# Optimization experiments

Measured on AMD Instinct MI355X. Metric: run time of the kernel, lower is better.

## Reference

```python
import jax, jax.numpy as jnp
import numpy as np

N = 100000      # nodes
E = 1600000     # edges
D = 128         # embedding_size (num_heads=1)
L = 4           # num_layers
NEG_SLOPE_ATT = 0.2    # GATConv attention LeakyReLU
NEG_SLOPE_ACT = 0.01   # nn.LeakyReLU default
LN_EPS = 1e-5


def leaky(x, s):
    return jnp.where(x > 0, x, s * x)


def layer_norm(x, gamma, beta):
    mu = jnp.mean(x, axis=-1, keepdims=True)
    var = jnp.mean(jnp.square(x - mu), axis=-1, keepdims=True)
    return (x - mu) * jax.lax.rsqrt(var + LN_EPS) * gamma + beta


def gat_conv(x, src, dst, W, a_src, a_dst, b):
    # PyG GATConv, heads=1, add_self_loops=False, no edge features
    h = x @ W                                  # [N, D]
    alpha_src = h @ a_src                      # [N]
    alpha_dst = h @ a_dst                      # [N]
    e = leaky(alpha_src[src] + alpha_dst[dst], NEG_SLOPE_ATT)   # [E]
    # softmax over incoming edges of each destination node
    m = jax.ops.segment_max(e, dst, num_segments=N)             # [N]
    ex = jnp.exp(e - m[dst])
    denom = jax.ops.segment_sum(ex, dst, num_segments=N)        # [N]
    alpha = ex / (denom[dst] + 1e-16)                           # [E]
    out = jax.ops.segment_sum(alpha[:, None] * h[src], dst, num_segments=N)
    return out + b


def setup_inputs() -> dict:
    key = jax.random.key(0)
    ks = jax.random.split(key, 12)
    x = jax.random.normal(ks[0], (N, D), dtype=jnp.float32)
    edge_index = jax.random.randint(ks[1], (2, E), 0, N, dtype=jnp.int32)
    s = 0.05
    return {
        "x": x,
        "edge_index": edge_index,
        "W_in": jax.random.normal(ks[2], (D, D), dtype=jnp.float32) * s,
        "b_in": jnp.zeros((D,), dtype=jnp.float32),
        "Wl": jax.random.normal(ks[3], (L, D, D), dtype=jnp.float32) * s,
        "att_src": jax.random.normal(ks[4], (L, D), dtype=jnp.float32) * s,
        "att_dst": jax.random.normal(ks[5], (L, D), dtype=jnp.float32) * s,
        "bias_l": jnp.zeros((L, D), dtype=jnp.float32),
        "gamma": jnp.ones((L, D), dtype=jnp.float32),
        "beta": jnp.zeros((L, D), dtype=jnp.float32),
    }


def reference(x, edge_index, W_in, b_in, Wl, att_src, att_dst, bias_l, gamma, beta):
    src, dst = edge_index[0], edge_index[1]
    h = leaky(x @ W_in + b_in, NEG_SLOPE_ACT)
    for i in range(L):
        h = gat_conv(h, src, dst, Wl[i], att_src[i], att_dst[i], bias_l[i])
        h = layer_norm(h, gamma[i], beta[i])
        h = leaky(h, NEG_SLOPE_ACT)
        # dropout p=0.3 is identity in eval mode; pooling undefined in source -> identity
    return h
```

## Files before the change

### kernel.cpp

```cpp
#include <hip/hip_runtime.h>
#include <hip/hip_fp16.h>
#include <math.h>

#define NN 100000
#define EE 1600000
#define DD 128
#define NBUCK 196
#define NBLKP 196
#define EPB 8192

typedef _Float16 f16;
typedef f16 f16x8 __attribute__((ext_vector_type(8)));
typedef float f32x4 __attribute__((ext_vector_type(4)));
typedef int int32x4 __attribute__((ext_vector_type(4)));

__device__ float llvm_amdgcn_raw_buffer_load_fp32(int32x4 srsrc, int voffset, int soffset,
                                                  int aux) __asm("llvm.amdgcn.raw.buffer.load.f32");

#define LDA 136
#define WCHUNKS 2304
#define WCOPY 2176

__global__ __launch_bounds__(256) void part_hist_k(const int* __restrict__ dst, int* __restrict__ bcnt) {
    __shared__ int lc[NBUCK];
    int t = threadIdx.x, blk = blockIdx.x;
    if (t < NBUCK) lc[t] = 0;
    __syncthreads();
    int e0 = blk * EPB;
    for (int i = t; i < EPB; i += 256) {
        int e = e0 + i;
        if (e < EE) atomicAdd(&lc[dst[e] >> 9], 1);
    }
    __syncthreads();
    if (t < NBUCK) bcnt[t * NBLKP + blk] = lc[t];
}

__global__ __launch_bounds__(256) void scanBB_k(const int* __restrict__ bcnt, int* __restrict__ ebase,
                                                int* __restrict__ btot) {
    __shared__ int sh[256];
    int t = threadIdx.x, b = blockIdx.x;
    int c = (t < NBLKP) ? bcnt[b * NBLKP + t] : 0;
    sh[t] = c;
    __syncthreads();
    for (int off = 1; off < 256; off <<= 1) {
        int v = (t >= off) ? sh[t - off] : 0;
        __syncthreads();
        sh[t] += v;
        __syncthreads();
    }
    if (t < NBLKP) ebase[b * NBLKP + t] = sh[t] - c;
    if (t == 255) btot[b] = sh[255];
}

__global__ __launch_bounds__(256) void scanBT_k(const int* __restrict__ btot, int* __restrict__ bstart,
                                                int* __restrict__ offsets) {
    __shared__ int sh[256];
    int t = threadIdx.x;
    int c = (t < NBUCK) ? btot[t] : 0;
    sh[t] = c;
    __syncthreads();
    for (int off = 1; off < 256; off <<= 1) {
        int v = (t >= off) ? sh[t - off] : 0;
        __syncthreads();
        sh[t] += v;
        __syncthreads();
    }
    if (t < NBUCK) bstart[t] = sh[t] - c;
    if (t == 0) { bstart[NBUCK] = EE; offsets[NN] = EE; }
}

__global__ __launch_bounds__(256) void part_k(const int* __restrict__ src, const int* __restrict__ dst,
                                              const int* __restrict__ bstart, const int* __restrict__ ebase,
                                              int2* __restrict__ ebuf) {
    __shared__ int cur[NBUCK];
    int t = threadIdx.x, blk = blockIdx.x;
    if (t < NBUCK) cur[t] = bstart[t] + ebase[t * NBLKP + blk];
    __syncthreads();
    int e0 = blk * EPB;
    for (int i = t; i < EPB; i += 256) {
        int e = e0 + i;
        if (e < EE) {
            int s = src[e], d = dst[e];
            int p = atomicAdd(&cur[d >> 9], 1);
            ebuf[p] = make_int2(s, d);
        }
    }
}

__global__ __launch_bounds__(512) void bucket_sort_k(const int2* __restrict__ ebuf,
                                                     const int* __restrict__ bstart,
                                                     int* __restrict__ offsets,
                                                     int* __restrict__ ssrc,
                                                     int* __restrict__ sdst) {
    __shared__ int sh[512];
    __shared__ int cur[512];
    int t = threadIdx.x, b = blockIdx.x;
    int d0 = b << 9;
    int beg = bstart[b], end = bstart[b + 1];

    cur[t] = 0;
    __syncthreads();
    for (int e = beg + t; e < end; e += 512) atomicAdd(&cur[ebuf[e].y - d0], 1);
    __syncthreads();
    int c = cur[t];
    sh[t] = c;
    __syncthreads();
    for (int off = 1; off < 512; off <<= 1) {
        int v = (t >= off) ? sh[t - off] : 0;
        __syncthreads();
        sh[t] += v;
        __syncthreads();
    }
    int excl = sh[t] - c;
    if (d0 + t < NN) offsets[d0 + t] = beg + excl;
    cur[t] = beg + excl;
    __syncthreads();
    for (int e = beg + t; e < end; e += 512) {
        int2 ed = ebuf[e];
        int p = atomicAdd(&cur[ed.y - d0], 1);
        ssrc[p] = ed.x;
        sdst[p] = ed.y;
    }
}

__global__ __launch_bounds__(256) void wprep_k(const float* __restrict__ W_in,
                                               const float* __restrict__ Wl,
                                               const float* __restrict__ att_src,
                                               const float* __restrict__ att_dst,
                                               f16* __restrict__ Wt,
                                               float* __restrict__ wav) {
    int m = blockIdx.x;
    const float* src = (m == 0) ? W_in : (Wl + (size_t)(m - 1) * DD * DD);
    f16* dst = Wt + (size_t)m * (WCHUNKS * 8);
    for (int q = 0; q < 64; ++q) {
        int idx = q * 256 + threadIdx.x;
        int k = idx >> 7, n = idx & 127;
        dst[n * LDA + k] = (f16)src[idx];
    }
    if (m >= 1) {
        int t = threadIdx.x;
        const float* av = (t < 128) ? (att_src + (size_t)(m - 1) * DD)
                                    : (att_dst + (size_t)(m - 1) * DD);
        int k = t & 127;
        float s = 0.f;
        for (int n = 0; n < 128; ++n) s += src[k * 128 + n] * av[n];
        wav[(size_t)(m - 1) * 256 + (t >> 7) * 128 + k] = s;
    }
}

__global__ __launch_bounds__(256, 2) void gemm_fused_k(const float* __restrict__ X,
                                                       const f16* __restrict__ Wt0,
                                                       const f16* __restrict__ Wt1,
                                                       const float* __restrict__ bias,
                                                       const float* __restrict__ wa_s,
                                                       const float* __restrict__ wa_d,
                                                       __half* __restrict__ Yh,
                                                       float* __restrict__ alpha_src,
                                                       float* __restrict__ alpha_dst) {
    __shared__ __align__(16) f16 sW[WCHUNKS * 8];
    __shared__ __align__(16) f16 sOut[4][32][LDA];
    int t = threadIdx.x;
    int w = t >> 6, lane = t & 63;
    int cl = lane & 15, qw = lane >> 4;
    int row0 = blockIdx.x * 128;

    f16x8 a[2][4];
#pragma unroll
    for (int rf = 0; rf < 2; ++rf) {
        int row = row0 + w * 32 + rf * 16 + cl;
        row = row < NN ? row : NN - 1;
        const float* p = X + (size_t)row * DD;
#pragma unroll
        for (int ks = 0; ks < 4; ++ks) {
            float4 u0 = *(const float4*)(p + ks * 32 + qw * 8);
            float4 u1 = *(const float4*)(p + ks * 32 + qw * 8 + 4);
            f16x8 v;
            v[0] = (f16)u0.x; v[1] = (f16)u0.y; v[2] = (f16)u0.z; v[3] = (f16)u0.w;
            v[4] = (f16)u1.x; v[5] = (f16)u1.y; v[6] = (f16)u1.z; v[7] = (f16)u1.w;
            a[rf][ks] = v;
        }
    }

    {
        const uint4* wsrc = (const uint4*)Wt0;
        uint4* wdst = (uint4*)sW;
#pragma unroll
        for (int it = 0; it < 9; ++it) wdst[it * 256 + t] = wsrc[it * 256 + t];
    }
    __syncthreads();

    f32x4 acc[2][8] = {};
#pragma unroll
    for (int ks = 0; ks < 4; ++ks) {
        int koff = ks * 32 + qw * 8;
#pragma unroll
        for (int nf = 0; nf < 8; ++nf) {
            f16x8 bh = *(const f16x8*)(sW + (nf * 16 + cl) * LDA + koff);
            acc[0][nf] = __builtin_amdgcn_mfma_f32_16x16x32_f16(a[0][ks], bh, acc[0][nf], 0, 0, 0);
            acc[1][nf] = __builtin_amdgcn_mfma_f32_16x16x32_f16(a[1][ks], bh, acc[1][nf], 0, 0, 0);
        }
    }

    __syncthreads();
    {
        const uint4* wsrc = (const uint4*)Wt1;
        uint4* wdst = (uint4*)sW;
#pragma unroll
        for (int it = 0; it < 9; ++it) wdst[it * 256 + t] = wsrc[it * 256 + t];
    }
    float bc[8];
#pragma unroll
    for (int nf = 0; nf < 8; ++nf) bc[nf] = bias[nf * 16 + cl];
#pragma unroll
    for (int rf = 0; rf < 2; ++rf)
#pragma unroll
        for (int i = 0; i < 4; ++i)
#pragma unroll
            for (int nf = 0; nf < 8; ++nf) {
                float v = acc[rf][nf][i] + bc[nf];
                v = v > 0.f ? v : 0.01f * v;
                sOut[w][rf * 16 + qw * 4 + i][nf * 16 + cl] = (f16)v;
            }
    __syncthreads();
#pragma unroll
    for (int rf = 0; rf < 2; ++rf)
#pragma unroll
        for (int ks = 0; ks < 4; ++ks)
            a[rf][ks] = *(const f16x8*)&sOut[w][rf * 16 + cl][ks * 32 + qw * 8];
#pragma unroll
    for (int rf = 0; rf < 2; ++rf)
#pragma unroll
        for (int nf = 0; nf < 8; ++nf)
            acc[rf][nf] = (f32x4){0.f, 0.f, 0.f, 0.f};
#pragma unroll
    for (int ks = 0; ks < 4; ++ks) {
        int koff = ks * 32 + qw * 8;
#pragma unroll
        for (int nf = 0; nf < 8; ++nf) {
            f16x8 bh = *(const f16x8*)(sW + (nf * 16 + cl) * LDA + koff);
            acc[0][nf] = __builtin_amdgcn_mfma_f32_16x16x32_f16(a[0][ks], bh, acc[0][nf], 0, 0, 0);
            acc[1][nf] = __builtin_amdgcn_mfma_f32_16x16x32_f16(a[1][ks], bh, acc[1][nf], 0, 0, 0);
        }
    }

#pragma unroll
    for (int rf = 0; rf < 2; ++rf) {
        float pa = 0.f, pb = 0.f;
#pragma unroll
        for (int ks = 0; ks < 4; ++ks) {
            const float* ps = wa_s + ks * 32 + qw * 8;
            const float* pd = wa_d + ks * 32 + qw * 8;
            float4 s0 = *(const float4*)ps, s1 = *(const float4*)(ps + 4);
            float4 d0 = *(const float4*)pd, d1 = *(const float4*)(pd + 4);
            float sv[8] = {s0.x, s0.y, s0.z, s0.w, s1.x, s1.y, s1.z, s1.w};
            float dv[8] = {d0.x, d0.y, d0.z, d0.w, d1.x, d1.y, d1.z, d1.w};
#pragma unroll
            for (int e = 0; e < 8; ++e) {
                float f = (float)a[rf][ks][e];
                pa = fmaf(f, sv[e], pa);
                pb = fmaf(f, dv[e], pb);
            }
        }
        pa += __shfl_xor(pa, 16); pa += __shfl_xor(pa, 32);
        pb += __shfl_xor(pb, 16); pb += __shfl_xor(pb, 32);
        if (qw == 0) {
            int row = row0 + w * 32 + rf * 16 + cl;
            if (row < NN) {
                alpha_src[row] = pa;
                alpha_dst[row] = pb;
            }
        }
    }

#pragma unroll
    for (int rf = 0; rf < 2; ++rf)
#pragma unroll
        for (int i = 0; i < 4; ++i)
#pragma unroll
            for (int nf = 0; nf < 8; ++nf)
                sOut[w][rf * 16 + qw * 4 + i][nf * 16 + cl] = (f16)acc[rf][nf][i];
#pragma unroll
    for (int p = 0; p < 8; ++p) {
        int rl = p * 4 + qw;
        uint4 v = *(const uint4*)&sOut[w][rl][cl * 8];
        int row = row0 + w * 32 + rl;
        if (row < NN) *(uint4*)(Yh + (size_t)row * DD + cl * 8) = v;
    }
}

__global__ __launch_bounds__(256, 3) void gemm_lite_k(const __half* __restrict__ Xh,
                                                      const f16* __restrict__ Wt0,
                                                      const float* __restrict__ wa_s,
                                                      const float* __restrict__ wa_d,
                                                      __half* __restrict__ Yh,
                                                      float* __restrict__ alpha_src,
                                                      float* __restrict__ alpha_dst) {
    __shared__ __align__(16) f16 sW[WCOPY * 8];
    __shared__ __align__(16) f16 sOut[4][16][LDA];
    int t = threadIdx.x;
    int w = t >> 6, lane = t & 63;
    int cl = lane & 15, qw = lane >> 4;
    int row0 = blockIdx.x * 128;

    const f16* X = (const f16*)Xh;
    f16x8 a[2][4];
#pragma unroll
    for (int rf = 0; rf < 2; ++rf) {
        int row = row0 + w * 32 + rf * 16 + cl;
        row = row < NN ? row : NN - 1;
        const f16* p = X + (size_t)row * DD;
#pragma unroll
        for (int ks = 0; ks < 4; ++ks)
            a[rf][ks] = *(const f16x8*)(p + ks * 32 + qw * 8);
    }

    {
        const uint4* wsrc = (const uint4*)Wt0;
        uint4* wdst = (uint4*)sW;
#pragma unroll
        for (int it = 0; it < 9; ++it) {
            int chunk = it * 256 + t;
            if (chunk < WCOPY) wdst[chunk] = wsrc[chunk];
        }
    }
    __syncthreads();

    f32x4 acc[2][8] = {};
#pragma unroll
    for (int ks = 0; ks < 4; ++ks) {
        int koff = ks * 32 + qw * 8;
#pragma unroll
        for (int nf = 0; nf < 8; ++nf) {
            f16x8 bh = *(const f16x8*)(sW + (nf * 16 + cl) * LDA + koff);
            acc[0][nf] = __builtin_amdgcn_mfma_f32_16x16x32_f16(a[0][ks], bh, acc[0][nf], 0, 0, 0);
            acc[1][nf] = __builtin_amdgcn_mfma_f32_16x16x32_f16(a[1][ks], bh, acc[1][nf], 0, 0, 0);
        }
    }

#pragma unroll
    for (int rf = 0; rf < 2; ++rf) {
        float pa = 0.f, pb = 0.f;
#pragma unroll
        for (int ks = 0; ks < 4; ++ks) {
            const float* ps = wa_s + ks * 32 + qw * 8;
            const float* pd = wa_d + ks * 32 + qw * 8;
            float4 s0 = *(const float4*)ps, s1 = *(const float4*)(ps + 4);
            float4 d0 = *(const float4*)pd, d1 = *(const float4*)(pd + 4);
            float sv[8] = {s0.x, s0.y, s0.z, s0.w, s1.x, s1.y, s1.z, s1.w};
            float dv[8] = {d0.x, d0.y, d0.z, d0.w, d1.x, d1.y, d1.z, d1.w};
#pragma unroll
            for (int e = 0; e < 8; ++e) {
                float f = (float)a[rf][ks][e];
                pa = fmaf(f, sv[e], pa);
                pb = fmaf(f, dv[e], pb);
            }
        }
        pa += __shfl_xor(pa, 16); pa += __shfl_xor(pa, 32);
        pb += __shfl_xor(pb, 16); pb += __shfl_xor(pb, 32);
        if (qw == 0) {
            int row = row0 + w * 32 + rf * 16 + cl;
            if (row < NN) {
                alpha_src[row] = pa;
                alpha_dst[row] = pb;
            }
        }
    }

#pragma unroll
    for (int rf = 0; rf < 2; ++rf) {
#pragma unroll
        for (int i = 0; i < 4; ++i)
#pragma unroll
            for (int nf = 0; nf < 8; ++nf)
                sOut[w][qw * 4 + i][nf * 16 + cl] = (f16)acc[rf][nf][i];
#pragma unroll
        for (int p = 0; p < 4; ++p) {
            int rl = p * 4 + qw;
            uint4 v = *(const uint4*)&sOut[w][rl][cl * 8];
            int row = row0 + w * 32 + rf * 16 + rl;
            if (row < NN) *(uint4*)(Yh + (size_t)row * DD + cl * 8) = v;
        }
    }
}

__global__ __launch_bounds__(256) void edgew_k(const int* __restrict__ ssrc,
                                               const int* __restrict__ sdst,
                                               const float* __restrict__ alpha_src,
                                               const float* __restrict__ alpha_dst,
                                               int2* __restrict__ epk) {
    int j = blockIdx.x * 256 + threadIdx.x;
    if (j < EE) {
        int s = ssrc[j];
        float e = alpha_src[s] + alpha_dst[sdst[j]];
        e = e > 0.f ? e : 0.2f * e;
        epk[j] = make_int2(s, __float_as_int(__expf(e)));
    } else if (j < EE + 16) {
        epk[j] = make_int2(0, 0);
    }
}

template <int HOUT>
__global__ __launch_bounds__(256) void agg_k(const __half* __restrict__ tmp,
                                             const int2* __restrict__ epk,
                                             const int* __restrict__ offsets,
                                             const float* __restrict__ bias,
                                             const float* __restrict__ gamma,
                                             const float* __restrict__ beta,
                                             void* __restrict__ outv) {
    int wid = (blockIdx.x * 256 + threadIdx.x) >> 6;
    wid = __builtin_amdgcn_readfirstlane(wid);
    int lane = threadIdx.x & 63;
    int beg = __builtin_amdgcn_readfirstlane(offsets[wid]);
    int end = __builtin_amdgcn_readfirstlane(offsets[wid + 1]);

    int32x4 rsrc;
    {
        unsigned long long b = (unsigned long long)(uintptr_t)tmp;
        rsrc.x = (int)(b & 0xffffffffull);
        rsrc.y = (int)(b >> 32);
        rsrc.z = NN * 256;
        rsrc.w = 0x00020000;
    }
    int voff = lane << 2;

    float ax0 = 0.f, ay0 = 0.f, ax1 = 0.f, ay1 = 0.f, dsum = 0.f;

    for (int j = (beg & ~1); j < end; j += 16) {
        int4 q[8];
#pragma unroll
        for (int k = 0; k < 8; ++k) q[k] = *(const int4*)(epk + j + 2 * k);
        float g[16];
#pragma unroll
        for (int k = 0; k < 8; ++k) {
            g[2 * k]     = llvm_amdgcn_raw_buffer_load_fp32(rsrc, voff, q[k].x << 8, 0);
            g[2 * k + 1] = llvm_amdgcn_raw_buffer_load_fp32(rsrc, voff, q[k].z << 8, 0);
        }
#pragma unroll
        for (int k = 0; k < 8; ++k) {
            int e0 = j + 2 * k, e1 = e0 + 1;
            bool v0 = (k == 0) ? (e0 >= beg && e0 < end) : (e0 < end);
            bool v1 = (e1 < end);
            float w0 = v0 ? __int_as_float(q[k].y) : 0.f;
            float w1 = v1 ? __int_as_float(q[k].w) : 0.f;
            union { float f; __half2 h; } u0, u1;
            u0.f = g[2 * k]; u1.f = g[2 * k + 1];
            dsum += w0 + w1;
            ax0 = fmaf(w0, __half2float(u0.h.x), ax0);
            ay0 = fmaf(w0, __half2float(u0.h.y), ay0);
            ax1 = fmaf(w1, __half2float(u1.h.x), ax1);
            ay1 = fmaf(w1, __half2float(u1.h.y), ay1);
        }
    }

    float inv = 1.0f / (dsum + 1e-16f);

    float ax = (ax0 + ax1) * inv + bias[2 * lane];
    float ay = (ay0 + ay1) * inv + bias[2 * lane + 1];

    float s1 = ax + ay;
#pragma unroll
    for (int off = 32; off >= 1; off >>= 1) s1 += __shfl_xor(s1, off);
    float mu = s1 * (1.0f / 128.0f);
    float dx = ax - mu, dy = ay - mu;
    float s2 = dx * dx + dy * dy;
#pragma unroll
    for (int off = 32; off >= 1; off >>= 1) s2 += __shfl_xor(s2, off);
    float rstd = rsqrtf(s2 * (1.0f / 128.0f) + 1e-5f);

    float yx = dx * rstd * gamma[2 * lane] + beta[2 * lane];
    float yy = dy * rstd * gamma[2 * lane + 1] + beta[2 * lane + 1];
    yx = yx > 0.f ? yx : 0.01f * yx;
    yy = yy > 0.f ? yy : 0.01f * yy;
    if (HOUT) {
        ((__half2*)outv)[(size_t)wid * 64 + lane] = __floats2half2_rn(yx, yy);
    } else {
        ((float2*)outv)[(size_t)wid * 64 + lane] = make_float2(yx, yy);
    }
}

extern "C" void kernel_launch(void* const* d_in, const int* in_sizes, int n_in,
                              void* d_out, int out_size, void* d_ws, size_t ws_size,
                              hipStream_t stream) {
    const float* x       = (const float*)d_in[0];
    const int*   ei      = (const int*)d_in[1];
    const float* W_in    = (const float*)d_in[2];
    const float* b_in    = (const float*)d_in[3];
    const float* Wl      = (const float*)d_in[4];
    const float* att_src = (const float*)d_in[5];
    const float* att_dst = (const float*)d_in[6];
    const float* bias_l  = (const float*)d_in[7];
    const float* gamma   = (const float*)d_in[8];
    const float* beta    = (const float*)d_in[9];
    float* out = (float*)d_out;

    char* ws = (char*)d_ws;
    __half* tmp      = (__half*)ws; ws += (size_t)NN * DD * 2;
    float* alpha_src = (float*)ws;  ws += (size_t)NN * 4;
    float* alpha_dst = (float*)ws;  ws += (size_t)NN * 4;
    int*   offsets   = (int*)ws;    ws += (size_t)(NN + 4) * 4;
    int*   ssrc      = (int*)ws;    ws += (size_t)EE * 4;
    int*   sdst      = (int*)ws;    ws += (size_t)EE * 4;
    int2*  ebuf      = (int2*)ws;   ws += (size_t)(EE + 16) * 8;
    int*   bcnt      = (int*)ws;    ws += (size_t)NBUCK * NBLKP * 4;
    int*   ebase     = (int*)ws;    ws += (size_t)NBUCK * NBLKP * 4;
    int*   btot      = (int*)ws;    ws += (size_t)(NBUCK + 4) * 4;
    int*   bstart    = (int*)ws;    ws += (size_t)(NBUCK + 4) * 4;
    f16*   Wt        = (f16*)ws;    ws += (size_t)5 * WCHUNKS * 16;
    float* wav       = (float*)ws;  ws += (size_t)4 * 256 * 4;
    int2* epk = ebuf;

    __half* hbuf = (__half*)d_out;

    const int* esrc = ei;
    const int* edst = ei + EE;

    part_hist_k<<<NBLKP, 256, 0, stream>>>(edst, bcnt);
    scanBB_k<<<NBUCK, 256, 0, stream>>>(bcnt, ebase, btot);
    scanBT_k<<<1, 256, 0, stream>>>(btot, bstart, offsets);
    part_k<<<NBLKP, 256, 0, stream>>>(esrc, edst, bstart, ebase, ebuf);
    bucket_sort_k<<<NBUCK, 512, 0, stream>>>(ebuf, bstart, offsets, ssrc, sdst);
    wprep_k<<<5, 256, 0, stream>>>(W_in, Wl, att_src, att_dst, Wt, wav);

    const int gg = (NN + 127) / 128;
    const int eg = (EE + 16 + 255) / 256;

    gemm_fused_k<<<gg, 256, 0, stream>>>(x, Wt, Wt + (size_t)1 * (WCHUNKS * 8), b_in,
                                         wav, wav + 128, tmp, alpha_src, alpha_dst);
    edgew_k<<<eg, 256, 0, stream>>>(ssrc, sdst, alpha_src, alpha_dst, epk);
    agg_k<1><<<NN / 4, 256, 0, stream>>>(tmp, epk, offsets, bias_l, gamma, beta, (void*)hbuf);

    for (int i = 1; i < 4; i++) {
        gemm_lite_k<<<gg, 256, 0, stream>>>(hbuf, Wt + (size_t)(i + 1) * (WCHUNKS * 8),
                                            wav + (size_t)i * 256, wav + (size_t)i * 256 + 128,
                                            tmp, alpha_src, alpha_dst);
        edgew_k<<<eg, 256, 0, stream>>>(ssrc, sdst, alpha_src, alpha_dst, epk);
        if (i < 3) {
            agg_k<1><<<NN / 4, 256, 0, stream>>>(tmp, epk, offsets,
                                                 bias_l + (size_t)i * DD, gamma + (size_t)i * DD,
                                                 beta + (size_t)i * DD, (void*)hbuf);
        } else {
            agg_k<0><<<NN / 4, 256, 0, stream>>>(tmp, epk, offsets,
                                                 bias_l + (size_t)i * DD, gamma + (size_t)i * DD,
                                                 beta + (size_t)i * DD, (void*)out);
        }
    }
}
```

Measured before the change: 545.3 us.

## Read weights directly from global in gemm_lite, vectorize edgew, deepen agg unroll

gemm_lite_k drops its shared-memory staging of the weight matrix and the block barrier, reading B fragments straight from global/L2. Each wave now handles 16 rows instead of 32, and launch bounds allow 4 blocks per CU. edgew_k processes two edges per thread with int2 loads and an int4 store, and the padding grows to 32 entries. agg_k unrolls to 32 edges per iteration to put more gathers in flight, at the cost of higher register pressure and possibly lower occupancy.

```diff
diff --git a/kernel.cpp b/kernel.cpp
--- a/kernel.cpp
+++ b/kernel.cpp
@@ -19,7 +19,6 @@
 
 #define LDA 136
 #define WCHUNKS 2304
-#define WCOPY 2176
 
 __global__ __launch_bounds__(256) void part_hist_k(const int* __restrict__ dst, int* __restrict__ bcnt) {
     __shared__ int lc[NBUCK];
@@ -288,57 +287,40 @@
     }
 }
 
-__global__ __launch_bounds__(256, 3) void gemm_lite_k(const __half* __restrict__ Xh,
+__global__ __launch_bounds__(256, 4) void gemm_lite_k(const __half* __restrict__ Xh,
                                                       const f16* __restrict__ Wt0,
                                                       const float* __restrict__ wa_s,
                                                       const float* __restrict__ wa_d,
                                                       __half* __restrict__ Yh,
                                                       float* __restrict__ alpha_src,
                                                       float* __restrict__ alpha_dst) {
-    __shared__ __align__(16) f16 sW[WCOPY * 8];
     __shared__ __align__(16) f16 sOut[4][16][LDA];
     int t = threadIdx.x;
     int w = t >> 6, lane = t & 63;
     int cl = lane & 15, qw = lane >> 4;
-    int row0 = blockIdx.x * 128;
+    int row0 = blockIdx.x * 64;
+    int row = row0 + w * 16 + cl;
+    int rowc = row < NN ? row : NN - 1;
 
     const f16* X = (const f16*)Xh;
-    f16x8 a[2][4];
-#pragma unroll
-    for (int rf = 0; rf < 2; ++rf) {
-        int row = row0 + w * 32 + rf * 16 + cl;
-        row = row < NN ? row : NN - 1;
-        const f16* p = X + (size_t)row * DD;
-#pragma unroll
-        for (int ks = 0; ks < 4; ++ks)
-            a[rf][ks] = *(const f16x8*)(p + ks * 32 + qw * 8);
+    const f16* p = X + (size_t)rowc * DD;
+    f16x8 a[4];
+#pragma unroll
+    for (int ks = 0; ks < 4; ++ks)
+        a[ks] = *(const f16x8*)(p + ks * 32 + qw * 8);
+
+    const f16* wp = Wt0 + cl * LDA + qw * 8;
+    f32x4 acc[8] = {};
+#pragma unroll
+    for (int ks = 0; ks < 4; ++ks) {
+#pragma unroll
+        for (int nf = 0; nf < 8; ++nf) {
+            f16x8 bh = *(const f16x8*)(wp + nf * (16 * LDA) + ks * 32);
+            acc[nf] = __builtin_amdgcn_mfma_f32_16x16x32_f16(a[ks], bh, acc[nf], 0, 0, 0);
+        }
     }
 
     {
-        const uint4* wsrc = (const uint4*)Wt0;
-        uint4* wdst = (uint4*)sW;
-#pragma unroll
-        for (int it = 0; it < 9; ++it) {
-            int chunk = it * 256 + t;
-            if (chunk < WCOPY) wdst[chunk] = wsrc[chunk];
-        }
-    }
-    __syncthreads();
-
-    f32x4 acc[2][8] = {};
-#pragma unroll
-    for (int ks = 0; ks < 4; ++ks) {
-        int koff = ks * 32 + qw * 8;
-#pragma unroll
-        for (int nf = 0; nf < 8; ++nf) {
-            f16x8 bh = *(const f16x8*)(sW + (nf * 16 + cl) * LDA + koff);
-            acc[0][nf] = __builtin_amdgcn_mfma_f32_16x16x32_f16(a[0][ks], bh, acc[0][nf], 0, 0, 0);
-            acc[1][nf] = __builtin_amdgcn_mfma_f32_16x16x32_f16(a[1][ks], bh, acc[1][nf], 0, 0, 0);
-        }
-    }
-
-#pragma unroll
-    for (int rf = 0; rf < 2; ++rf) {
         float pa = 0.f, pb = 0.f;
 #pragma unroll
         for (int ks = 0; ks < 4; ++ks) {
@@ -350,36 +332,30 @@
             float dv[8] = {d0.x, d0.y, d0.z, d0.w, d1.x, d1.y, d1.z, d1.w};
 #pragma unroll
             for (int e = 0; e < 8; ++e) {
-                float f = (float)a[rf][ks][e];
+                float f = (float)a[ks][e];
                 pa = fmaf(f, sv[e], pa);
                 pb = fmaf(f, dv[e], pb);
             }
         }
         pa += __shfl_xor(pa, 16); pa += __shfl_xor(pa, 32);
         pb += __shfl_xor(pb, 16); pb += __shfl_xor(pb, 32);
-        if (qw == 0) {
-            int row = row0 + w * 32 + rf * 16 + cl;
-            if (row < NN) {
-                alpha_src[row] = pa;
-                alpha_dst[row] = pb;
-            }
-        }
-    }
-
-#pragma unroll
-    for (int rf = 0; rf < 2; ++rf) {
-#pragma unroll
-        for (int i = 0; i < 4; ++i)
-#pragma unroll
-            for (int nf = 0; nf < 8; ++nf)
-                sOut[w][qw * 4 + i][nf * 16 + cl] = (f16)acc[rf][nf][i];
-#pragma unroll
-        for (int p = 0; p < 4; ++p) {
-            int rl = p * 4 + qw;
-            uint4 v = *(const uint4*)&sOut[w][rl][cl * 8];
-            int row = row0 + w * 32 + rf * 16 + rl;
-            if (row < NN) *(uint4*)(Yh + (size_t)row * DD + cl * 8) = v;
-        }
+        if (qw == 0 && row < NN) {
+            alpha_src[row] = pa;
+            alpha_dst[row] = pb;
+        }
+    }
+
+#pragma unroll
+    for (int i = 0; i < 4; ++i)
+#pragma unroll
+        for (int nf = 0; nf < 8; ++nf)
+            sOut[w][qw * 4 + i][nf * 16 + cl] = (f16)acc[nf][i];
+#pragma unroll
+    for (int pp = 0; pp < 4; ++pp) {
+        int rl = pp * 4 + qw;
+        uint4 v = *(const uint4*)&sOut[w][rl][cl * 8];
+        int row2 = row0 + w * 16 + rl;
+        if (row2 < NN) *(uint4*)(Yh + (size_t)row2 * DD + cl * 8) = v;
     }
 }
 
@@ -388,14 +364,21 @@
                                                const float* __restrict__ alpha_src,
                                                const float* __restrict__ alpha_dst,
                                                int2* __restrict__ epk) {
-    int j = blockIdx.x * 256 + threadIdx.x;
-    if (j < EE) {
-        int s = ssrc[j];
-        float e = alpha_src[s] + alpha_dst[sdst[j]];
-        e = e > 0.f ? e : 0.2f * e;
-        epk[j] = make_int2(s, __float_as_int(__expf(e)));
-    } else if (j < EE + 16) {
-        epk[j] = make_int2(0, 0);
+    int j2 = blockIdx.x * 256 + threadIdx.x;
+    int e0 = j2 * 2;
+    if (e0 < EE) {
+        int2 s2 = *(const int2*)(ssrc + e0);
+        int2 d2 = *(const int2*)(sdst + e0);
+        float ea = alpha_src[s2.x] + alpha_dst[d2.x];
+        float eb = alpha_src[s2.y] + alpha_dst[d2.y];
+        ea = ea > 0.f ? ea : 0.2f * ea;
+        eb = eb > 0.f ? eb : 0.2f * eb;
+        int4 rec;
+        rec.x = s2.x; rec.y = __float_as_int(__expf(ea));
+        rec.z = s2.y; rec.w = __float_as_int(__expf(eb));
+        *(int4*)(epk + e0) = rec;
+    } else if (e0 < EE + 32) {
+        *(int4*)(epk + e0) = make_int4(0, 0, 0, 0);
     }
 }
 
@@ -425,18 +408,18 @@
 
     float ax0 = 0.f, ay0 = 0.f, ax1 = 0.f, ay1 = 0.f, dsum = 0.f;
 
-    for (int j = (beg & ~1); j < end; j += 16) {
-        int4 q[8];
-#pragma unroll
-        for (int k = 0; k < 8; ++k) q[k] = *(const int4*)(epk + j + 2 * k);
-        float g[16];
-#pragma unroll
-        for (int k = 0; k < 8; ++k) {
+    for (int j = (beg & ~1); j < end; j += 32) {
+        int4 q[16];
+#pragma unroll
+        for (int k = 0; k < 16; ++k) q[k] = *(const int4*)(epk + j + 2 * k);
+        float g[32];
+#pragma unroll
+        for (int k = 0; k < 16; ++k) {
             g[2 * k]     = llvm_amdgcn_raw_buffer_load_fp32(rsrc, voff, q[k].x << 8, 0);
             g[2 * k + 1] = llvm_amdgcn_raw_buffer_load_fp32(rsrc, voff, q[k].z << 8, 0);
         }
 #pragma unroll
-        for (int k = 0; k < 8; ++k) {
+        for (int k = 0; k < 16; ++k) {
             int e0 = j + 2 * k, e1 = e0 + 1;
             bool v0 = (k == 0) ? (e0 >= beg && e0 < end) : (e0 < end);
             bool v1 = (e1 < end);
@@ -500,7 +483,7 @@
     int*   offsets   = (int*)ws;    ws += (size_t)(NN + 4) * 4;
     int*   ssrc      = (int*)ws;    ws += (size_t)EE * 4;
     int*   sdst      = (int*)ws;    ws += (size_t)EE * 4;
-    int2*  ebuf      = (int2*)ws;   ws += (size_t)(EE + 16) * 8;
+    int2*  ebuf      = (int2*)ws;   ws += (size_t)(EE + 32) * 8;
     int*   bcnt      = (int*)ws;    ws += (size_t)NBUCK * NBLKP * 4;
     int*   ebase     = (int*)ws;    ws += (size_t)NBUCK * NBLKP * 4;
     int*   btot      = (int*)ws;    ws += (size_t)(NBUCK + 4) * 4;
@@ -521,8 +504,9 @@
     bucket_sort_k<<<NBUCK, 512, 0, stream>>>(ebuf, bstart, offsets, ssrc, sdst);
     wprep_k<<<5, 256, 0, stream>>>(W_in, Wl, att_src, att_dst, Wt, wav);
 
-    const int gg = (NN + 127) / 128;
-    const int eg = (EE + 16 + 255) / 256;
+    const int gg  = (NN + 127) / 128;
+    const int gg2 = (NN + 63) / 64;
+    const int eg  = (EE / 2 + 16 + 255) / 256;
 
     gemm_fused_k<<<gg, 256, 0, stream>>>(x, Wt, Wt + (size_t)1 * (WCHUNKS * 8), b_in,
                                          wav, wav + 128, tmp, alpha_src, alpha_dst);
@@ -530,9 +514,9 @@
     agg_k<1><<<NN / 4, 256, 0, stream>>>(tmp, epk, offsets, bias_l, gamma, beta, (void*)hbuf);
 
     for (int i = 1; i < 4; i++) {
-        gemm_lite_k<<<gg, 256, 0, stream>>>(hbuf, Wt + (size_t)(i + 1) * (WCHUNKS * 8),
-                                            wav + (size_t)i * 256, wav + (size_t)i * 256 + 128,
-                                            tmp, alpha_src, alpha_dst);
+        gemm_lite_k<<<gg2, 256, 0, stream>>>(hbuf, Wt + (size_t)(i + 1) * (WCHUNKS * 8),
+                                             wav + (size_t)i * 256, wav + (size_t)i * 256 + 128,
+                                             tmp, alpha_src, alpha_dst);
         edgew_k<<<eg, 256, 0, stream>>>(ssrc, sdst, alpha_src, alpha_dst, epk);
         if (i < 3) {
             agg_k<1><<<NN / 4, 256, 0, stream>>>(tmp, epk, offsets,
```

Measured after the change: 583.5 us. 1.07x slower.
